# Performance work log

Hardware: AMD Instinct MI355X
Metric: run time of the kernel (lower is better)

## Reference

```python
import jax, jax.numpy as jnp
import numpy as np

NU, NV, E = 20000, 20000, 320000
CU, CV, CE = 256, 256, 64
OU, OV, OE = 256, 256, 64
EPS = 1e-5


def seg_mean(x, idx, n):
    s = jax.ops.segment_sum(x, idx, num_segments=n)
    cnt = jax.ops.segment_sum(jnp.ones((x.shape[0],), x.dtype), idx, num_segments=n)
    return s / jnp.maximum(cnt, 1.0)[:, None]


def seg_max(x, idx, n):
    m = jax.ops.segment_max(x, idx, num_segments=n)
    return jnp.where(jnp.isfinite(m), m, jnp.zeros_like(m))  # empty segments -> 0 (torch_sparse behavior)


def batchnorm(x, gamma, beta):
    mu = x.mean(axis=0)
    var = ((x - mu) ** 2).mean(axis=0)  # biased, as in torch BN training
    return (x - mu) * jax.lax.rsqrt(var + EPS) * gamma + beta


def setup_inputs() -> dict:
    key = jax.random.key(0)
    ks = jax.random.split(key, 24)
    inp = {
        'xus': jax.random.normal(ks[0], (NU, CU), jnp.float32),
        'xut': jax.random.normal(ks[1], (NU, CU), jnp.float32),
        'xvs': jax.random.normal(ks[2], (NV, CV), jnp.float32),
        'xvt': jax.random.normal(ks[3], (NV, CV), jnp.float32),
        'xe_e': jax.random.normal(ks[4], (E, CE), jnp.float32),
        'xe_v2u': jax.random.normal(ks[5], (E, CE), jnp.float32),
        'xe_u2v': jax.random.normal(ks[6], (E, CE), jnp.float32),
        'row_v2u': jax.random.randint(ks[7], (E,), 0, NU, jnp.int32),
        'col_v2u': jax.random.randint(ks[8], (E,), 0, NV, jnp.int32),
        'row_u2v': jax.random.randint(ks[9], (E,), 0, NU, jnp.int32),
        'col_u2v': jax.random.randint(ks[10], (E,), 0, NV, jnp.int32),
        'row_e': jax.random.randint(ks[11], (E,), 0, NU, jnp.int32),
        'col_e': jax.random.randint(ks[12], (E,), 0, NV, jnp.int32),
    }
    d_in_u = CU + 2 * CV + 2 * CE  # self + mean/max(v) + mean/max(e)
    d_in_v = 2 * CU + CV + 2 * CE
    d_in_e = CU + CV + CE
    sc = lambda n: 1.0 / np.sqrt(n)
    inp['attn_v2u'] = jax.random.normal(ks[13], (CV, 1), jnp.float32) * sc(CV)
    inp['W_v2u'] = jax.random.normal(ks[14], (d_in_u, OU), jnp.float32) * sc(d_in_u)
    inp['b_v2u'] = jnp.zeros((OU,), jnp.float32)
    inp['g_v2u'] = jnp.ones((OU,), jnp.float32)
    inp['be_v2u'] = jnp.zeros((OU,), jnp.float32)
    inp['attn_u2v'] = jax.random.normal(ks[15], (CV, 1), jnp.float32) * sc(CV)
    inp['W_u2v'] = jax.random.normal(ks[16], (d_in_v, OV), jnp.float32) * sc(d_in_v)
    inp['b_u2v'] = jnp.zeros((OV,), jnp.float32)
    inp['g_u2v'] = jnp.ones((OV,), jnp.float32)
    inp['be_u2v'] = jnp.zeros((OV,), jnp.float32)
    inp['W_e'] = jax.random.normal(ks[17], (d_in_e, OE), jnp.float32) * sc(d_in_e)
    inp['b_e'] = jnp.zeros((OE,), jnp.float32)
    inp['g_e'] = jnp.ones((OE,), jnp.float32)
    inp['be_e'] = jnp.zeros((OE,), jnp.float32)
    return inp


def reference(xus, xut, xvs, xvt, xe_e, xe_v2u, xe_u2v,
              row_v2u, col_v2u, row_u2v, col_u2v, row_e, col_e,
              attn_v2u, W_v2u, b_v2u, g_v2u, be_v2u,
              attn_u2v, W_u2v, b_u2v, g_u2v, be_u2v,
              W_e, b_e, g_e, be_e):
    nu, nv = xut.shape[0], xvt.shape[0]
    # ---- v->u conv: attention over ALL v source nodes (global softmax) ----
    aw_v = jax.nn.softmax((xvs @ attn_v2u).squeeze(-1), axis=0)[:, None]  # [Nv,1]
    xw_v = aw_v * xvs
    msg_v = xw_v[col_v2u]  # [E,CV] gather
    mean_v = seg_mean(msg_v, row_v2u, nu)
    max_v = seg_max(msg_v, row_v2u, nu)
    mean_ev = seg_mean(xe_v2u, row_v2u, nu)
    max_ev = seg_max(xe_v2u, row_v2u, nu)
    h_u = jnp.concatenate((xut, mean_v, max_v, mean_ev, max_ev), axis=1)
    out_u = batchnorm(h_u @ W_v2u + b_v2u, g_v2u, be_v2u)
    # ---- u->v conv ----
    aw_u = jax.nn.softmax((xus @ attn_u2v).squeeze(-1), axis=0)[:, None]  # [Nu,1]
    xw_u = aw_u * xus
    msg_u = xw_u[row_u2v]  # [E,CU]
    mean_u = seg_mean(msg_u, col_u2v, nv)
    max_u = seg_max(msg_u, col_u2v, nv)
    mean_eu = seg_mean(xe_u2v, col_u2v, nv)
    max_eu = seg_max(xe_u2v, col_u2v, nv)
    h_v = jnp.concatenate((xvt, mean_u, max_u, mean_eu, max_eu), axis=1)
    out_v = batchnorm(h_v @ W_u2v + b_u2v, g_u2v, be_u2v)
    # ---- edge conv: gather endpoints, concat, linear, bn ----
    h_e = jnp.concatenate((xe_e, xut[row_e], xvt[col_e]), axis=1)  # [E, CE+CU+CV]
    out_e = batchnorm(h_e @ W_e + b_e, g_e, be_e)
    return (out_u, out_v, out_e)
```

## Files before the change

### kernel.cpp

```cpp
#include <hip/hip_runtime.h>
#include <stdint.h>

#define N_U 20000
#define N_V 20000
#define N_E 320000
#define EPS_F 1e-5f
#define NEG_HUGE -3.402823466e38f

using bf16x8 = __attribute__((__ext_vector_type__(8))) __bf16;
using f32x4  = __attribute__((__ext_vector_type__(4))) float;

__device__ __forceinline__ unsigned short f2bf(float f) {
  unsigned int u = __float_as_uint(f);
  u += 0x7FFFu + ((u >> 16) & 1u);
  return (unsigned short)(u >> 16);
}

__device__ __forceinline__ ushort4 bf4(float4 v) {
  return make_ushort4(f2bf(v.x), f2bf(v.y), f2bf(v.z), f2bf(v.w));
}

__global__ void k_logits2(const float* __restrict__ xus, const float* __restrict__ xvs,
                          const float* __restrict__ attn_u2v, const float* __restrict__ attn_v2u,
                          float* __restrict__ logits_u, float* __restrict__ logits_v) {
  int wid = (blockIdx.x * 256 + threadIdx.x) >> 6;
  int lane = threadIdx.x & 63;
  bool isU = wid < N_U;
  int node = isU ? wid : wid - N_U;
  const float4* x4 = reinterpret_cast<const float4*>(isU ? xus : xvs);
  const float4* a4 = reinterpret_cast<const float4*>(isU ? attn_u2v : attn_v2u);
  float4 xv = x4[(size_t)node * 64 + lane];
  float4 av = a4[lane];
  float s = xv.x * av.x + xv.y * av.y + xv.z * av.z + xv.w * av.w;
#pragma unroll
  for (int o = 32; o; o >>= 1) s += __shfl_down(s, o);
  if (lane == 0) (isU ? logits_u : logits_v)[node] = s;
}

__global__ void k_softmax_stat(const float* __restrict__ lu, const float* __restrict__ lv,
                               float* __restrict__ stat, int n) {
  const float* l = blockIdx.x ? lv : lu;
  float* st = stat + (blockIdx.x ? 4 : 0);
  __shared__ float red[16];
  __shared__ float sm;
  int t = threadIdx.x;
  float m = NEG_HUGE;
  for (int i = t; i < n; i += 1024) m = fmaxf(m, l[i]);
#pragma unroll
  for (int o = 32; o; o >>= 1) m = fmaxf(m, __shfl_down(m, o));
  if ((t & 63) == 0) red[t >> 6] = m;
  __syncthreads();
  if (t == 0) {
    float mm = red[0];
    for (int i = 1; i < 16; i++) mm = fmaxf(mm, red[i]);
    sm = mm;
  }
  __syncthreads();
  float mx = sm;
  float s = 0.f;
  for (int i = t; i < n; i += 1024) s += __expf(l[i] - mx);
#pragma unroll
  for (int o = 32; o; o >>= 1) s += __shfl_down(s, o);
  __syncthreads();
  if ((t & 63) == 0) red[t >> 6] = s;
  __syncthreads();
  if (t == 0) {
    float ss = 0.f;
    for (int i = 0; i < 16; i++) ss += red[i];
    st[0] = mx;
    st[1] = ss;
  }
}

__global__ void k_hist2(const int* __restrict__ d0, int* __restrict__ c0,
                        const int* __restrict__ d1, int* __restrict__ c1) {
  int b = blockIdx.x;
  if (b < 1250) atomicAdd(&c0[d0[b * 256 + threadIdx.x]], 1);
  else atomicAdd(&c1[d1[(b - 1250) * 256 + threadIdx.x]], 1);
}

__global__ void k_scan2(const int* __restrict__ cnt0, int* __restrict__ off0, int* __restrict__ cur0,
                        const int* __restrict__ cnt1, int* __restrict__ off1, int* __restrict__ cur1,
                        int n) {
  const int* cnt = blockIdx.x ? cnt1 : cnt0;
  int* off = blockIdx.x ? off1 : off0;
  int* cur = blockIdx.x ? cur1 : cur0;
  __shared__ int warpsum[16];
  __shared__ int carry;
  int t = threadIdx.x;
  if (t == 0) carry = 0;
  __syncthreads();
  for (int base = 0; base < n; base += 1024) {
    int i = base + t;
    int v = (i < n) ? cnt[i] : 0;
    int lane = t & 63, w = t >> 6;
    int incl = v;
#pragma unroll
    for (int o = 1; o < 64; o <<= 1) {
      int u = __shfl_up(incl, o);
      if (lane >= o) incl += u;
    }
    if (lane == 63) warpsum[w] = incl;
    __syncthreads();
    if (t == 0) {
      int s = 0;
      for (int k = 0; k < 16; k++) { int x = warpsum[k]; warpsum[k] = s; s += x; }
    }
    __syncthreads();
    int excl = incl - v + warpsum[w] + carry;
    if (i < n) { off[i] = excl; cur[i] = excl; }
    __syncthreads();
    if (t == 1023) carry = excl + v;
    __syncthreads();
  }
  if (t == 0) off[n] = carry;
}

__global__ void k_scatter2(const int* __restrict__ d0, const int* __restrict__ s0,
                           int* __restrict__ cur0, int2* __restrict__ p0,
                           const int* __restrict__ d1, const int* __restrict__ s1,
                           int* __restrict__ cur1, int2* __restrict__ p1) {
  int b = blockIdx.x;
  if (b < 1250) {
    int e = b * 256 + threadIdx.x;
    int p = atomicAdd(&cur0[d0[e]], 1);
    p0[p] = make_int2(e, s0[e]);
  } else {
    int e = (b - 1250) * 256 + threadIdx.x;
    int p = atomicAdd(&cur1[d1[e]], 1);
    p1[p] = make_int2(e, s1[e]);
  }
}

__global__ __launch_bounds__(256) void k_agg(
    const float* __restrict__ xvs, const float* __restrict__ xus,
    const float* __restrict__ logits_v, const float* __restrict__ logits_u,
    const float* __restrict__ smstat,
    const float* __restrict__ xe_v2u, const float* __restrict__ xe_u2v,
    const int* __restrict__ off_u, const int* __restrict__ off_v,
    const int2* __restrict__ perm_u, const int2* __restrict__ perm_v,
    const float* __restrict__ xut, const float* __restrict__ xvt,
    unsigned short* __restrict__ h_u, unsigned short* __restrict__ h_v) {
  int wid = (blockIdx.x * 256 + threadIdx.x) >> 6;
  int lane = threadIdx.x & 63;
  bool isU = wid < N_U;
  int node = isU ? wid : wid - N_U;
  const float4* xsrc4 = reinterpret_cast<const float4*>(isU ? xvs : xus);
  const float* lg = isU ? logits_v : logits_u;
  float mx = smstat[isU ? 4 : 0];
  float inv_se = 1.f / smstat[isU ? 5 : 1];
  const float* xe = isU ? xe_v2u : xe_u2v;
  const int* off = isU ? off_u : off_v;
  const int2* perm = isU ? perm_u : perm_v;
  const float4* xt4 = reinterpret_cast<const float4*>(isU ? xut : xvt);
  unsigned short* h = isU ? h_u : h_v;

  int beg = off[node], end = off[node + 1];
  float4 s = {0.f, 0.f, 0.f, 0.f};
  float4 m4 = {NEG_HUGE, NEG_HUGE, NEG_HUGE, NEG_HUGE};
  float se = 0.f, me = NEG_HUGE;

  for (int c = beg; c < end; c += 64) {
    int n = end - c;
    n = n > 64 ? 64 : n;
    int2 pe = perm[c + (lane < n ? lane : 0)];
    float av = __expf(lg[pe.y] - mx) * inv_se;
    int j = 0;
    for (; j + 4 <= n; j += 4) {
      int ey0 = __shfl(pe.y, j + 0), ex0 = __shfl(pe.x, j + 0); float a0 = __shfl(av, j + 0);
      int ey1 = __shfl(pe.y, j + 1), ex1 = __shfl(pe.x, j + 1); float a1 = __shfl(av, j + 1);
      int ey2 = __shfl(pe.y, j + 2), ex2 = __shfl(pe.x, j + 2); float a2 = __shfl(av, j + 2);
      int ey3 = __shfl(pe.y, j + 3), ex3 = __shfl(pe.x, j + 3); float a3 = __shfl(av, j + 3);
      float4 v0 = xsrc4[(size_t)ey0 * 64 + lane];
      float4 v1 = xsrc4[(size_t)ey1 * 64 + lane];
      float4 v2 = xsrc4[(size_t)ey2 * 64 + lane];
      float4 v3 = xsrc4[(size_t)ey3 * 64 + lane];
      float e0 = xe[(size_t)ex0 * 64 + lane];
      float e1 = xe[(size_t)ex1 * 64 + lane];
      float e2 = xe[(size_t)ex2 * 64 + lane];
      float e3 = xe[(size_t)ex3 * 64 + lane];
      float4 w0 = {a0 * v0.x, a0 * v0.y, a0 * v0.z, a0 * v0.w};
      float4 w1 = {a1 * v1.x, a1 * v1.y, a1 * v1.z, a1 * v1.w};
      float4 w2 = {a2 * v2.x, a2 * v2.y, a2 * v2.z, a2 * v2.w};
      float4 w3 = {a3 * v3.x, a3 * v3.y, a3 * v3.z, a3 * v3.w};
      s.x += w0.x + w1.x + w2.x + w3.x;
      s.y += w0.y + w1.y + w2.y + w3.y;
      s.z += w0.z + w1.z + w2.z + w3.z;
      s.w += w0.w + w1.w + w2.w + w3.w;
      m4.x = fmaxf(fmaxf(fmaxf(m4.x, w0.x), fmaxf(w1.x, w2.x)), w3.x);
      m4.y = fmaxf(fmaxf(fmaxf(m4.y, w0.y), fmaxf(w1.y, w2.y)), w3.y);
      m4.z = fmaxf(fmaxf(fmaxf(m4.z, w0.z), fmaxf(w1.z, w2.z)), w3.z);
      m4.w = fmaxf(fmaxf(fmaxf(m4.w, w0.w), fmaxf(w1.w, w2.w)), w3.w);
      se += e0 + e1 + e2 + e3;
      me = fmaxf(fmaxf(fmaxf(me, e0), fmaxf(e1, e2)), e3);
    }
    for (; j < n; j++) {
      int ey = __shfl(pe.y, j), ex = __shfl(pe.x, j);
      float a = __shfl(av, j);
      float4 v = xsrc4[(size_t)ey * 64 + lane];
      float ev = xe[(size_t)ex * 64 + lane];
      s.x += a * v.x; s.y += a * v.y; s.z += a * v.z; s.w += a * v.w;
      m4.x = fmaxf(m4.x, a * v.x); m4.y = fmaxf(m4.y, a * v.y);
      m4.z = fmaxf(m4.z, a * v.z); m4.w = fmaxf(m4.w, a * v.w);
      se += ev; me = fmaxf(me, ev);
    }
  }

  int deg = end - beg;
  float inv = 1.f / (float)(deg > 0 ? deg : 1);
  size_t hb = (size_t)node * 896;
  ushort4* h4 = reinterpret_cast<ushort4*>(h + hb);
  float4 self = xt4[(size_t)node * 64 + lane];
  h4[lane] = bf4(self);
  h4[64 + lane] = bf4(make_float4(s.x * inv, s.y * inv, s.z * inv, s.w * inv));
  float4 mo = deg > 0 ? m4 : make_float4(0.f, 0.f, 0.f, 0.f);
  h4[128 + lane] = bf4(mo);
  h[hb + 768 + lane] = f2bf(se * inv);
  h[hb + 832 + lane] = f2bf(deg > 0 ? me : 0.f);
}

__global__ void k_wt_all(const float* __restrict__ W0, const float* __restrict__ W1,
                         const float* __restrict__ W2, unsigned short* __restrict__ T0,
                         unsigned short* __restrict__ T1, unsigned short* __restrict__ T2) {
  int i = blockIdx.x * 256 + threadIdx.x;
  const float* W;
  unsigned short* T;
  int K, N;
  if (i < 229376) { W = W0; T = T0; K = 896; N = 256; }
  else if (i < 458752) { i -= 229376; W = W1; T = T1; K = 896; N = 256; }
  else { i -= 458752; if (i >= 36864) return; W = W2; T = T2; K = 576; N = 64; }
  int k = i / N, n = i % N;
  T[(size_t)n * K + k] = f2bf(W[i]);
}

template <int TN, bool STATS>
__global__ __launch_bounds__(256) void k_gemm(
    const unsigned short* __restrict__ A0, const unsigned short* __restrict__ A1, int lda,
    const unsigned short* __restrict__ B0, const unsigned short* __restrict__ B1, int ldb,
    float* __restrict__ C0, float* __restrict__ C1, int ldc, int M, int K,
    float* __restrict__ sum0, float* __restrict__ sum1,
    float* __restrict__ sq0, float* __restrict__ sq1) {
  constexpr int WAVES_N = TN / 64;
  constexpr int WAVES_M = 4 / WAVES_N;
  constexpr int WTM = 128 / WAVES_M;
  constexpr int MT = WTM / 16;
  constexpr int NT = 4;
  constexpr int LS = 56;

  __shared__ __align__(16) unsigned short As[128 * LS];
  __shared__ __align__(16) unsigned short Bs[TN * LS];
  __shared__ float ssum[TN], ssq[TN];

  const unsigned short* A = blockIdx.z ? A1 : A0;
  const unsigned short* B = blockIdx.z ? B1 : B0;
  float* C = blockIdx.z ? C1 : C0;
  float* sum = blockIdx.z ? sum1 : sum0;
  float* sq = blockIdx.z ? sq1 : sq0;

  const int t = threadIdx.x;
  const int m0 = blockIdx.x * 128;
  const int n0 = blockIdx.y * TN;
  const int lane = t & 63;
  const int w = t >> 6;
  const int wm = w % WAVES_M;
  const int wn = w / WAVES_M;

  if (STATS && t < TN) { ssum[t] = 0.f; ssq[t] = 0.f; }

  f32x4 acc[MT][NT];
#pragma unroll
  for (int i = 0; i < MT; i++)
#pragma unroll
    for (int j = 0; j < NT; j++) acc[i][j] = (f32x4){0.f, 0.f, 0.f, 0.f};

  const int arow_l = wm * WTM + (lane & 15);
  const int koff_l = (lane >> 4) * 8;

  for (int k0 = 0; k0 < K; k0 += 32) {
    if (k0) __syncthreads();
#pragma unroll
    for (int p = 0; p < 2; p++) {
      int c = t + p * 256;
      int row = c >> 2, kc = c & 3;
      int rg = m0 + row;
      rg = rg < M ? rg : M - 1;
      *reinterpret_cast<uint4*>(&As[row * LS + kc * 8]) =
          *reinterpret_cast<const uint4*>(A + (size_t)rg * lda + k0 + kc * 8);
    }
#pragma unroll
    for (int p = 0; p < TN / 64; p++) {
      int c = t + p * 256;
      int row = c >> 2, kc = c & 3;
      *reinterpret_cast<uint4*>(&Bs[row * LS + kc * 8]) =
          *reinterpret_cast<const uint4*>(B + (size_t)(n0 + row) * ldb + k0 + kc * 8);
    }
    __syncthreads();
    bf16x8 af[MT], bfv[NT];
#pragma unroll
    for (int i = 0; i < MT; i++)
      af[i] = *reinterpret_cast<const bf16x8*>(&As[(arow_l + i * 16) * LS + koff_l]);
#pragma unroll
    for (int j = 0; j < NT; j++)
      bfv[j] = *reinterpret_cast<const bf16x8*>(&Bs[(wn * 64 + j * 16 + (lane & 15)) * LS + koff_l]);
#pragma unroll
    for (int i = 0; i < MT; i++)
#pragma unroll
      for (int j = 0; j < NT; j++)
        acc[i][j] = __builtin_amdgcn_mfma_f32_16x16x32_bf16(af[i], bfv[j], acc[i][j], 0, 0, 0);
  }

  float st[NT], qt[NT];
#pragma unroll
  for (int j = 0; j < NT; j++) { st[j] = 0.f; qt[j] = 0.f; }
#pragma unroll
  for (int i = 0; i < MT; i++) {
#pragma unroll
    for (int j = 0; j < NT; j++) {
      int col = n0 + wn * 64 + j * 16 + (lane & 15);
#pragma unroll
      for (int r = 0; r < 4; r++) {
        int row = m0 + wm * WTM + i * 16 + (lane >> 4) * 4 + r;
        if (row < M) {
          float v = acc[i][j][r];
          C[(size_t)row * ldc + col] = v;
          if (STATS) { st[j] += v; qt[j] += v * v; }
        }
      }
    }
  }
  if (STATS) {
#pragma unroll
    for (int j = 0; j < NT; j++) {
      st[j] += __shfl_xor(st[j], 16); st[j] += __shfl_xor(st[j], 32);
      qt[j] += __shfl_xor(qt[j], 16); qt[j] += __shfl_xor(qt[j], 32);
    }
    if (lane < 16) {
#pragma unroll
      for (int j = 0; j < NT; j++) {
        atomicAdd(&ssum[wn * 64 + j * 16 + lane], st[j]);
        atomicAdd(&ssq[wn * 64 + j * 16 + lane], qt[j]);
      }
    }
    __syncthreads();
    if (t < TN) {
      atomicAdd(&sum[n0 + t], ssum[t]);
      atomicAdd(&sq[n0 + t], ssq[t]);
    }
  }
}

__global__ __launch_bounds__(256) void k_gemm_e(
    const float* __restrict__ xe_e, const unsigned short* __restrict__ Wt,
    const int* __restrict__ rowe, const int* __restrict__ cole,
    const float* __restrict__ pu, const float* __restrict__ pv,
    float* __restrict__ OutE, float* __restrict__ sum, float* __restrict__ sq) {
  constexpr int LSB = 72;
  __shared__ __align__(16) unsigned short Bs[64 * LSB];
  __shared__ float ssum[64], ssq[64];
  int t = threadIdx.x;
  int lane = t & 63, w = t >> 6;
  if (t < 64) { ssum[t] = 0.f; ssq[t] = 0.f; }
  {
    int row = t >> 2, seg = t & 3;
    const uint4* src = reinterpret_cast<const uint4*>(Wt + (size_t)row * 576 + seg * 16);
    uint4* dst = reinterpret_cast<uint4*>(&Bs[row * LSB + seg * 16]);
    dst[0] = src[0];
    dst[1] = src[1];
  }
  __syncthreads();

  int m0 = blockIdx.x * 128;
  f32x4 acc[2][4];
#pragma unroll
  for (int i = 0; i < 2; i++)
#pragma unroll
    for (int j = 0; j < 4; j++) acc[i][j] = (f32x4){0.f, 0.f, 0.f, 0.f};

#pragma unroll
  for (int k0 = 0; k0 < 64; k0 += 32) {
    bf16x8 af[2], bfv[4];
#pragma unroll
    for (int i = 0; i < 2; i++) {
      int row = m0 + w * 32 + i * 16 + (lane & 15);
      const float4* ap = reinterpret_cast<const float4*>(xe_e + (size_t)row * 64 + k0 + (lane >> 4) * 8);
      float4 a0 = ap[0], a1 = ap[1];
      union { bf16x8 v; ushort4 u[2]; } pk;
      pk.u[0] = bf4(a0);
      pk.u[1] = bf4(a1);
      af[i] = pk.v;
    }
#pragma unroll
    for (int j = 0; j < 4; j++)
      bfv[j] = *reinterpret_cast<const bf16x8*>(&Bs[(j * 16 + (lane & 15)) * LSB + k0 + (lane >> 4) * 8]);
#pragma unroll
    for (int i = 0; i < 2; i++)
#pragma unroll
      for (int j = 0; j < 4; j++)
        acc[i][j] = __builtin_amdgcn_mfma_f32_16x16x32_bf16(af[i], bfv[j], acc[i][j], 0, 0, 0);
  }

  float st[4] = {0.f, 0.f, 0.f, 0.f}, qt[4] = {0.f, 0.f, 0.f, 0.f};
#pragma unroll
  for (int i = 0; i < 2; i++) {
    int base = m0 + w * 32 + i * 16 + (lane >> 4) * 4;
#pragma unroll
    for (int r = 0; r < 4; r++) {
      int e = base + r;
      int ru = rowe[e], cv = cole[e];
      const float* pur = pu + (size_t)ru * 64;
      const float* pvr = pv + (size_t)cv * 64;
#pragma unroll
      for (int j = 0; j < 4; j++) {
        int col = j * 16 + (lane & 15);
        float v = acc[i][j][r] + pur[col] + pvr[col];
        OutE[(size_t)e * 64 + col] = v;
        st[j] += v;
        qt[j] += v * v;
      }
    }
  }
#pragma unroll
  for (int j = 0; j < 4; j++) {
    st[j] += __shfl_xor(st[j], 16); st[j] += __shfl_xor(st[j], 32);
    qt[j] += __shfl_xor(qt[j], 16); qt[j] += __shfl_xor(qt[j], 32);
  }
  if (lane < 16) {
#pragma unroll
    for (int j = 0; j < 4; j++) {
      atomicAdd(&ssum[j * 16 + lane], st[j]);
      atomicAdd(&ssq[j * 16 + lane], qt[j]);
    }
  }
  __syncthreads();
  if (t < 64) {
    atomicAdd(&sum[t], ssum[t]);
    atomicAdd(&sq[t], ssq[t]);
  }
}

__global__ void k_bn4(float* __restrict__ out_u, float* __restrict__ out_v,
                      float* __restrict__ out_e, const float* __restrict__ stats,
                      const float* __restrict__ g_u, const float* __restrict__ be_u,
                      const float* __restrict__ g_v, const float* __restrict__ be_v,
                      const float* __restrict__ g_e, const float* __restrict__ be_e) {
  int b = blockIdx.x;
  float* X;
  const float *sum, *sq, *g, *be;
  int cmask;
  float invn;
  long base;
  if (b < 5000) {
    X = out_u; base = (long)b * 1024; sum = stats; sq = stats + 256;
    g = g_u; be = be_u; cmask = 255; invn = 1.f / N_U;
  } else if (b < 10000) {
    X = out_v; base = (long)(b - 5000) * 1024; sum = stats + 512; sq = stats + 768;
    g = g_v; be = be_v; cmask = 255; invn = 1.f / N_V;
  } else {
    X = out_e; base = (long)(b - 10000) * 1024; sum = stats + 1024; sq = stats + 1088;
    g = g_e; be = be_e; cmask = 63; invn = 1.f / N_E;
  }
  long i4 = base + (long)threadIdx.x * 4;
  int c0 = (int)(i4 & cmask);
  float4 v = *reinterpret_cast<float4*>(X + i4);
  float r[4] = {v.x, v.y, v.z, v.w};
#pragma unroll
  for (int k = 0; k < 4; k++) {
    int c = c0 + k;
    float mu = sum[c] * invn;
    float var = sq[c] * invn - mu * mu;
    r[k] = (r[k] - mu) * rsqrtf(var + EPS_F) * g[c] + be[c];
  }
  *reinterpret_cast<float4*>(X + i4) = make_float4(r[0], r[1], r[2], r[3]);
}

extern "C" void kernel_launch(void* const* d_in, const int* in_sizes, int n_in, void* d_out,
                              int out_size, void* d_ws, size_t ws_size, hipStream_t stream) {
  (void)in_sizes; (void)n_in; (void)out_size; (void)ws_size;
  const float* xus = (const float*)d_in[0];
  const float* xut = (const float*)d_in[1];
  const float* xvs = (const float*)d_in[2];
  const float* xvt = (const float*)d_in[3];
  const float* xe_e = (const float*)d_in[4];
  const float* xe_v2u = (const float*)d_in[5];
  const float* xe_u2v = (const float*)d_in[6];
  const int* row_v2u = (const int*)d_in[7];
  const int* col_v2u = (const int*)d_in[8];
  const int* row_u2v = (const int*)d_in[9];
  const int* col_u2v = (const int*)d_in[10];
  const int* row_e = (const int*)d_in[11];
  const int* col_e = (const int*)d_in[12];
  const float* W_v2u = (const float*)d_in[14];
  const float* g_v2u = (const float*)d_in[16];
  const float* be_v2u = (const float*)d_in[17];
  const float* W_u2v = (const float*)d_in[19];
  const float* g_u2v = (const float*)d_in[21];
  const float* be_u2v = (const float*)d_in[22];
  const float* W_e = (const float*)d_in[23];
  const float* g_e = (const float*)d_in[25];
  const float* be_e = (const float*)d_in[26];
  const float* attn_v2u = (const float*)d_in[13];
  const float* attn_u2v = (const float*)d_in[18];

  char* p = (char*)d_ws;
  auto alloc = [&](size_t bytes) {
    char* r = p;
    p += (bytes + 15) & ~(size_t)15;
    return r;
  };
  int* cnt_u = (int*)alloc(N_U * 4);
  int* cnt_v = (int*)alloc(N_V * 4);
  float* stats = (float*)alloc(1152 * 4);
  size_t zero_bytes = (size_t)(p - (char*)d_ws);
  int* off_u = (int*)alloc((N_U + 1) * 4);
  int* cur_u = (int*)alloc(N_U * 4);
  int2* perm_u = (int2*)alloc((size_t)N_E * 8);
  int* off_v = (int*)alloc((N_V + 1) * 4);
  int* cur_v = (int*)alloc(N_V * 4);
  int2* perm_v = (int2*)alloc((size_t)N_E * 8);
  float* logits_u = (float*)alloc(N_U * 4);
  float* logits_v = (float*)alloc(N_V * 4);
  float* smstat = (float*)alloc(8 * 4);
  unsigned short* h_u = (unsigned short*)alloc((size_t)N_U * 896 * 2);
  unsigned short* h_v = (unsigned short*)alloc((size_t)N_V * 896 * 2);
  unsigned short* Wt_v2u = (unsigned short*)alloc((size_t)896 * 256 * 2);
  unsigned short* Wt_u2v = (unsigned short*)alloc((size_t)896 * 256 * 2);
  unsigned short* Wt_e = (unsigned short*)alloc((size_t)576 * 64 * 2);
  float* pu = (float*)alloc((size_t)N_U * 64 * 4);
  float* pv = (float*)alloc((size_t)N_V * 64 * 4);

  float* out_u = (float*)d_out;
  float* out_v = out_u + (size_t)N_U * 256;
  float* out_e = out_v + (size_t)N_V * 256;

  hipMemsetAsync(d_ws, 0, zero_bytes, stream);

  k_logits2<<<10000, 256, 0, stream>>>(xus, xvs, attn_u2v, attn_v2u, logits_u, logits_v);
  k_softmax_stat<<<2, 1024, 0, stream>>>(logits_u, logits_v, smstat, N_U);
  k_hist2<<<2500, 256, 0, stream>>>(row_v2u, cnt_u, col_u2v, cnt_v);
  k_scan2<<<2, 1024, 0, stream>>>(cnt_u, off_u, cur_u, cnt_v, off_v, cur_v, N_U);
  k_scatter2<<<2500, 256, 0, stream>>>(row_v2u, col_v2u, cur_u, perm_u, col_u2v, row_u2v, cur_v, perm_v);
  k_agg<<<10000, 256, 0, stream>>>(xvs, xus, logits_v, logits_u, smstat, xe_v2u, xe_u2v,
                                   off_u, off_v, perm_u, perm_v, xut, xvt, h_u, h_v);
  k_wt_all<<<1936, 256, 0, stream>>>(W_v2u, W_u2v, W_e, Wt_v2u, Wt_u2v, Wt_e);

  k_gemm<128, true><<<dim3(157, 2, 2), 256, 0, stream>>>(
      h_u, h_v, 896, Wt_v2u, Wt_u2v, 896, out_u, out_v, 256, N_U, 896,
      stats, stats + 512, stats + 256, stats + 768);
  k_gemm<64, false><<<dim3(157, 1, 2), 256, 0, stream>>>(
      h_u, h_v, 896, Wt_e + 64, Wt_e + 320, 576, pu, pv, 64, N_U, 256,
      nullptr, nullptr, nullptr, nullptr);
  k_gemm_e<<<2500, 256, 0, stream>>>(xe_e, Wt_e, row_e, col_e, pu, pv, out_e,
                                     stats + 1024, stats + 1088);
  k_bn4<<<30000, 256, 0, stream>>>(out_u, out_v, out_e, stats, g_v2u, be_v2u,
                                   g_u2v, be_u2v, g_e, be_e);
}
```

Baseline: 706.0 us.

## Precompute bf16 attention-weighted node features before gather aggregation; tile weight transpose

Adds a pre-pass kernel that applies the softmax attention weight to each source node once, stores the result as bf16, and writes the self features into h. The aggregation kernel then gathers half-width bf16 rows instead of fp32 rows and no longer recomputes exp per edge. Edge-feature loads become nontemporal. The weight transpose now goes through a shared-memory tile so both its reads and writes are coalesced. In exchange the messages are rounded to bf16 before summation rather than after, which changes numerics slightly, and there is an extra kernel launch plus an extra intermediate buffer.

```diff
diff --git a/kernel.cpp b/kernel.cpp
--- a/kernel.cpp
+++ b/kernel.cpp
@@ -14,6 +14,10 @@
   unsigned int u = __float_as_uint(f);
   u += 0x7FFFu + ((u >> 16) & 1u);
   return (unsigned short)(u >> 16);
+}
+
+__device__ __forceinline__ float b2f(unsigned short u) {
+  return __uint_as_float((unsigned int)u << 16);
 }
 
 __device__ __forceinline__ ushort4 bf4(float4 v) {
@@ -70,6 +74,33 @@
     st[0] = mx;
     st[1] = ss;
   }
+}
+
+__global__ void k_preweight(const float* __restrict__ xus, const float* __restrict__ xvs,
+                            const float* __restrict__ xut, const float* __restrict__ xvt,
+                            const float* __restrict__ logits_u, const float* __restrict__ logits_v,
+                            const float* __restrict__ smstat,
+                            unsigned short* __restrict__ xw_u, unsigned short* __restrict__ xw_v,
+                            unsigned short* __restrict__ h_u, unsigned short* __restrict__ h_v) {
+  int wid = (blockIdx.x * 256 + threadIdx.x) >> 6;
+  int lane = threadIdx.x & 63;
+  bool isU = wid < N_U;
+  int node = isU ? wid : wid - N_U;
+  const float4* xs4 = reinterpret_cast<const float4*>(isU ? xus : xvs);
+  const float4* xt4 = reinterpret_cast<const float4*>(isU ? xut : xvt);
+  const float* lg = isU ? logits_u : logits_v;
+  float mx = smstat[isU ? 0 : 4];
+  float ise = 1.f / smstat[isU ? 1 : 5];
+  unsigned short* xw = isU ? xw_u : xw_v;
+  unsigned short* h = isU ? h_u : h_v;
+
+  float a = __expf(lg[node] - mx) * ise;
+  float4 xv = xs4[(size_t)node * 64 + lane];
+  ushort4* xw4 = reinterpret_cast<ushort4*>(xw + (size_t)node * 256);
+  xw4[lane] = bf4(make_float4(a * xv.x, a * xv.y, a * xv.z, a * xv.w));
+  float4 tv = xt4[(size_t)node * 64 + lane];
+  ushort4* h4 = reinterpret_cast<ushort4*>(h + (size_t)node * 896);
+  h4[lane] = bf4(tv);
 }
 
 __global__ void k_hist2(const int* __restrict__ d0, int* __restrict__ c0,
@@ -133,26 +164,19 @@
 }
 
 __global__ __launch_bounds__(256) void k_agg(
-    const float* __restrict__ xvs, const float* __restrict__ xus,
-    const float* __restrict__ logits_v, const float* __restrict__ logits_u,
-    const float* __restrict__ smstat,
+    const unsigned short* __restrict__ xw_v, const unsigned short* __restrict__ xw_u,
     const float* __restrict__ xe_v2u, const float* __restrict__ xe_u2v,
     const int* __restrict__ off_u, const int* __restrict__ off_v,
     const int2* __restrict__ perm_u, const int2* __restrict__ perm_v,
-    const float* __restrict__ xut, const float* __restrict__ xvt,
     unsigned short* __restrict__ h_u, unsigned short* __restrict__ h_v) {
   int wid = (blockIdx.x * 256 + threadIdx.x) >> 6;
   int lane = threadIdx.x & 63;
   bool isU = wid < N_U;
   int node = isU ? wid : wid - N_U;
-  const float4* xsrc4 = reinterpret_cast<const float4*>(isU ? xvs : xus);
-  const float* lg = isU ? logits_v : logits_u;
-  float mx = smstat[isU ? 4 : 0];
-  float inv_se = 1.f / smstat[isU ? 5 : 1];
+  const ushort4* xw4 = reinterpret_cast<const ushort4*>(isU ? xw_v : xw_u);
   const float* xe = isU ? xe_v2u : xe_u2v;
   const int* off = isU ? off_u : off_v;
   const int2* perm = isU ? perm_u : perm_v;
-  const float4* xt4 = reinterpret_cast<const float4*>(isU ? xut : xvt);
   unsigned short* h = isU ? h_u : h_v;
 
   int beg = off[node], end = off[node + 1];
@@ -164,44 +188,43 @@
     int n = end - c;
     n = n > 64 ? 64 : n;
     int2 pe = perm[c + (lane < n ? lane : 0)];
-    float av = __expf(lg[pe.y] - mx) * inv_se;
     int j = 0;
     for (; j + 4 <= n; j += 4) {
-      int ey0 = __shfl(pe.y, j + 0), ex0 = __shfl(pe.x, j + 0); float a0 = __shfl(av, j + 0);
-      int ey1 = __shfl(pe.y, j + 1), ex1 = __shfl(pe.x, j + 1); float a1 = __shfl(av, j + 1);
-      int ey2 = __shfl(pe.y, j + 2), ex2 = __shfl(pe.x, j + 2); float a2 = __shfl(av, j + 2);
-      int ey3 = __shfl(pe.y, j + 3), ex3 = __shfl(pe.x, j + 3); float a3 = __shfl(av, j + 3);
-      float4 v0 = xsrc4[(size_t)ey0 * 64 + lane];
-      float4 v1 = xsrc4[(size_t)ey1 * 64 + lane];
-      float4 v2 = xsrc4[(size_t)ey2 * 64 + lane];
-      float4 v3 = xsrc4[(size_t)ey3 * 64 + lane];
-      float e0 = xe[(size_t)ex0 * 64 + lane];
-      float e1 = xe[(size_t)ex1 * 64 + lane];
-      float e2 = xe[(size_t)ex2 * 64 + lane];
-      float e3 = xe[(size_t)ex3 * 64 + lane];
-      float4 w0 = {a0 * v0.x, a0 * v0.y, a0 * v0.z, a0 * v0.w};
-      float4 w1 = {a1 * v1.x, a1 * v1.y, a1 * v1.z, a1 * v1.w};
-      float4 w2 = {a2 * v2.x, a2 * v2.y, a2 * v2.z, a2 * v2.w};
-      float4 w3 = {a3 * v3.x, a3 * v3.y, a3 * v3.z, a3 * v3.w};
-      s.x += w0.x + w1.x + w2.x + w3.x;
-      s.y += w0.y + w1.y + w2.y + w3.y;
-      s.z += w0.z + w1.z + w2.z + w3.z;
-      s.w += w0.w + w1.w + w2.w + w3.w;
-      m4.x = fmaxf(fmaxf(fmaxf(m4.x, w0.x), fmaxf(w1.x, w2.x)), w3.x);
-      m4.y = fmaxf(fmaxf(fmaxf(m4.y, w0.y), fmaxf(w1.y, w2.y)), w3.y);
-      m4.z = fmaxf(fmaxf(fmaxf(m4.z, w0.z), fmaxf(w1.z, w2.z)), w3.z);
-      m4.w = fmaxf(fmaxf(fmaxf(m4.w, w0.w), fmaxf(w1.w, w2.w)), w3.w);
+      int ey0 = __shfl(pe.y, j + 0), ex0 = __shfl(pe.x, j + 0);
+      int ey1 = __shfl(pe.y, j + 1), ex1 = __shfl(pe.x, j + 1);
+      int ey2 = __shfl(pe.y, j + 2), ex2 = __shfl(pe.x, j + 2);
+      int ey3 = __shfl(pe.y, j + 3), ex3 = __shfl(pe.x, j + 3);
+      ushort4 u0 = xw4[(size_t)ey0 * 64 + lane];
+      ushort4 u1 = xw4[(size_t)ey1 * 64 + lane];
+      ushort4 u2 = xw4[(size_t)ey2 * 64 + lane];
+      ushort4 u3 = xw4[(size_t)ey3 * 64 + lane];
+      float e0 = __builtin_nontemporal_load(xe + (size_t)ex0 * 64 + lane);
+      float e1 = __builtin_nontemporal_load(xe + (size_t)ex1 * 64 + lane);
+      float e2 = __builtin_nontemporal_load(xe + (size_t)ex2 * 64 + lane);
+      float e3 = __builtin_nontemporal_load(xe + (size_t)ex3 * 64 + lane);
+      float w0x = b2f(u0.x), w0y = b2f(u0.y), w0z = b2f(u0.z), w0w = b2f(u0.w);
+      float w1x = b2f(u1.x), w1y = b2f(u1.y), w1z = b2f(u1.z), w1w = b2f(u1.w);
+      float w2x = b2f(u2.x), w2y = b2f(u2.y), w2z = b2f(u2.z), w2w = b2f(u2.w);
+      float w3x = b2f(u3.x), w3y = b2f(u3.y), w3z = b2f(u3.z), w3w = b2f(u3.w);
+      s.x += w0x + w1x + w2x + w3x;
+      s.y += w0y + w1y + w2y + w3y;
+      s.z += w0z + w1z + w2z + w3z;
+      s.w += w0w + w1w + w2w + w3w;
+      m4.x = fmaxf(fmaxf(fmaxf(m4.x, w0x), fmaxf(w1x, w2x)), w3x);
+      m4.y = fmaxf(fmaxf(fmaxf(m4.y, w0y), fmaxf(w1y, w2y)), w3y);
+      m4.z = fmaxf(fmaxf(fmaxf(m4.z, w0z), fmaxf(w1z, w2z)), w3z);
+      m4.w = fmaxf(fmaxf(fmaxf(m4.w, w0w), fmaxf(w1w, w2w)), w3w);
       se += e0 + e1 + e2 + e3;
       me = fmaxf(fmaxf(fmaxf(me, e0), fmaxf(e1, e2)), e3);
     }
     for (; j < n; j++) {
       int ey = __shfl(pe.y, j), ex = __shfl(pe.x, j);
-      float a = __shfl(av, j);
-      float4 v = xsrc4[(size_t)ey * 64 + lane];
-      float ev = xe[(size_t)ex * 64 + lane];
-      s.x += a * v.x; s.y += a * v.y; s.z += a * v.z; s.w += a * v.w;
-      m4.x = fmaxf(m4.x, a * v.x); m4.y = fmaxf(m4.y, a * v.y);
-      m4.z = fmaxf(m4.z, a * v.z); m4.w = fmaxf(m4.w, a * v.w);
+      ushort4 u0 = xw4[(size_t)ey * 64 + lane];
+      float ev = __builtin_nontemporal_load(xe + (size_t)ex * 64 + lane);
+      float wx = b2f(u0.x), wy = b2f(u0.y), wz = b2f(u0.z), ww = b2f(u0.w);
+      s.x += wx; s.y += wy; s.z += wz; s.w += ww;
+      m4.x = fmaxf(m4.x, wx); m4.y = fmaxf(m4.y, wy);
+      m4.z = fmaxf(m4.z, wz); m4.w = fmaxf(m4.w, ww);
       se += ev; me = fmaxf(me, ev);
     }
   }
@@ -210,8 +233,6 @@
   float inv = 1.f / (float)(deg > 0 ? deg : 1);
   size_t hb = (size_t)node * 896;
   ushort4* h4 = reinterpret_cast<ushort4*>(h + hb);
-  float4 self = xt4[(size_t)node * 64 + lane];
-  h4[lane] = bf4(self);
   h4[64 + lane] = bf4(make_float4(s.x * inv, s.y * inv, s.z * inv, s.w * inv));
   float4 mo = deg > 0 ? m4 : make_float4(0.f, 0.f, 0.f, 0.f);
   h4[128 + lane] = bf4(mo);
@@ -219,18 +240,33 @@
   h[hb + 832 + lane] = f2bf(deg > 0 ? me : 0.f);
 }
 
-__global__ void k_wt_all(const float* __restrict__ W0, const float* __restrict__ W1,
-                         const float* __restrict__ W2, unsigned short* __restrict__ T0,
-                         unsigned short* __restrict__ T1, unsigned short* __restrict__ T2) {
-  int i = blockIdx.x * 256 + threadIdx.x;
+__global__ void k_wt_tiled(const float* __restrict__ W0, const float* __restrict__ W1,
+                           const float* __restrict__ W2, unsigned short* __restrict__ T0,
+                           unsigned short* __restrict__ T1, unsigned short* __restrict__ T2) {
+  __shared__ unsigned short tile[64][66];
+  int b = blockIdx.x;
   const float* W;
   unsigned short* T;
   int K, N;
-  if (i < 229376) { W = W0; T = T0; K = 896; N = 256; }
-  else if (i < 458752) { i -= 229376; W = W1; T = T1; K = 896; N = 256; }
-  else { i -= 458752; if (i >= 36864) return; W = W2; T = T2; K = 576; N = 64; }
-  int k = i / N, n = i % N;
-  T[(size_t)n * K + k] = f2bf(W[i]);
+  if (b < 56) { W = W0; T = T0; K = 896; N = 256; }
+  else if (b < 112) { b -= 56; W = W1; T = T1; K = 896; N = 256; }
+  else { b -= 112; W = W2; T = T2; K = 576; N = 64; }
+  int ntn = N >> 6;
+  int k0 = (b / ntn) << 6, n0 = (b % ntn) << 6;
+  int t = threadIdx.x;
+#pragma unroll
+  for (int i = 0; i < 16; i++) {
+    int idx = t + i * 256;
+    int k = idx >> 6, n = idx & 63;
+    tile[k][n] = f2bf(W[(size_t)(k0 + k) * N + n0 + n]);
+  }
+  __syncthreads();
+#pragma unroll
+  for (int i = 0; i < 16; i++) {
+    int idx = t + i * 256;
+    int n = idx >> 6, k = idx & 63;
+    T[(size_t)(n0 + n) * K + k0 + k] = tile[k][n];
+  }
 }
 
 template <int TN, bool STATS>
@@ -527,6 +563,8 @@
   unsigned short* Wt_e = (unsigned short*)alloc((size_t)576 * 64 * 2);
   float* pu = (float*)alloc((size_t)N_U * 64 * 4);
   float* pv = (float*)alloc((size_t)N_V * 64 * 4);
+  unsigned short* xw_u = (unsigned short*)alloc((size_t)N_U * 256 * 2);
+  unsigned short* xw_v = (unsigned short*)alloc((size_t)N_V * 256 * 2);
 
   float* out_u = (float*)d_out;
   float* out_v = out_u + (size_t)N_U * 256;
@@ -536,12 +574,14 @@
 
   k_logits2<<<10000, 256, 0, stream>>>(xus, xvs, attn_u2v, attn_v2u, logits_u, logits_v);
   k_softmax_stat<<<2, 1024, 0, stream>>>(logits_u, logits_v, smstat, N_U);
+  k_preweight<<<10000, 256, 0, stream>>>(xus, xvs, xut, xvt, logits_u, logits_v, smstat,
+                                         xw_u, xw_v, h_u, h_v);
   k_hist2<<<2500, 256, 0, stream>>>(row_v2u, cnt_u, col_u2v, cnt_v);
   k_scan2<<<2, 1024, 0, stream>>>(cnt_u, off_u, cur_u, cnt_v, off_v, cur_v, N_U);
   k_scatter2<<<2500, 256, 0, stream>>>(row_v2u, col_v2u, cur_u, perm_u, col_u2v, row_u2v, cur_v, perm_v);
-  k_agg<<<10000, 256, 0, stream>>>(xvs, xus, logits_v, logits_u, smstat, xe_v2u, xe_u2v,
-                                   off_u, off_v, perm_u, perm_v, xut, xvt, h_u, h_v);
-  k_wt_all<<<1936, 256, 0, stream>>>(W_v2u, W_u2v, W_e, Wt_v2u, Wt_u2v, Wt_e);
+  k_agg<<<10000, 256, 0, stream>>>(xw_v, xw_u, xe_v2u, xe_u2v,
+                                   off_u, off_v, perm_u, perm_v, h_u, h_v);
+  k_wt_tiled<<<121, 256, 0, stream>>>(W_v2u, W_u2v, W_e, Wt_v2u, Wt_u2v, Wt_e);
 
   k_gemm<128, true><<<dim3(157, 2, 2), 256, 0, stream>>>(
       h_u, h_v, 896, Wt_v2u, Wt_u2v, 896, out_u, out_v, 256, N_U, 896,
```

After: 673.8 us. -4.6%, faster.
